# Performance work log

Measured on AMD Instinct MI355X. Metric: run time of the kernel, lower is better.

Reference implementation:

```python
import jax, jax.numpy as jnp
import numpy as np

EMBED_DIM = 256
NUM_EMBEDDINGS = 1024
COMMITMENT_COST = 0.25


def setup_inputs() -> dict:
    key = jax.random.key(0)
    k1, k2 = jax.random.split(key)
    z_e = jax.random.normal(k1, (64, 32, 32, EMBED_DIM), dtype=jnp.float32)
    # variance_scaling(fan_in, uniform) ~ U(-sqrt(3/fan_in), sqrt(3/fan_in))
    lim = float(np.sqrt(3.0 / EMBED_DIM))
    codebook = jax.random.uniform(k2, (NUM_EMBEDDINGS, EMBED_DIM), dtype=jnp.float32,
                                  minval=-lim, maxval=lim)
    return {"z_e": z_e, "codebook": codebook}


def reference(z_e, codebook):
    codebook = jnp.asarray(codebook, dtype=jnp.float32)
    z_flat = jnp.reshape(z_e, (-1, codebook.shape[1]))  # [N, D]
    # ||z||^2 - 2 z.c + ||c||^2 -> [N, K]
    distances = (jnp.sum(z_flat ** 2, axis=1, keepdims=True)
                 - 2.0 * jnp.dot(z_flat, codebook.T)
                 + jnp.sum(codebook ** 2, axis=1))
    encoding_indices = jnp.argmin(distances, axis=1)  # [N]
    quantized = jnp.reshape(codebook[encoding_indices], z_e.shape)
    commitment_loss = COMMITMENT_COST * jnp.mean((jax.lax.stop_gradient(quantized) - z_e) ** 2)
    embedding_loss = jnp.mean((quantized - jax.lax.stop_gradient(z_e)) ** 2)
    quantized = z_e + jax.lax.stop_gradient(quantized - z_e)  # straight-through
    return (quantized, commitment_loss, embedding_loss, encoding_indices)
```

## Files before the change

### kernel.cpp

```cpp
#include <hip/hip_runtime.h>

#define NROWS  65536
#define DIM    256
#define KCB    1024
#define DELTA  0.012f
#define DELTA2 2.0e-4f
#define NRMAX  65536

typedef __attribute__((ext_vector_type(8))) _Float16 v8h;
typedef __attribute__((ext_vector_type(4))) float v4f;
typedef __attribute__((ext_vector_type(4))) int   v4i;

__device__ __forceinline__ unsigned short h16(float x) {
  _Float16 h = (_Float16)x;
  return __builtin_bit_cast(unsigned short, h);
}
__device__ __forceinline__ unsigned pk2h(float a, float b) {
  return (unsigned)h16(a) | ((unsigned)h16(b) << 16);
}
__device__ __forceinline__ v4i pk8h(float4 a, float4 b) {
  v4i r; r.x = (int)pk2h(a.x,a.y); r.y = (int)pk2h(a.z,a.w);
  r.z = (int)pk2h(b.x,b.y); r.w = (int)pk2h(b.z,b.w);
  return r;
}
__device__ __forceinline__ float f16f(float x) { return (float)(_Float16)x; }
__device__ __forceinline__ void gld16(const void* g, void* l) {
  __builtin_amdgcn_global_load_lds(
      (const __attribute__((address_space(1))) unsigned int*)g,
      (__attribute__((address_space(3))) unsigned int*)l, 16, 0, 0);
}

__global__ __launch_bounds__(256) void prep_kernel(const float* __restrict__ cb,
                                                   float* __restrict__ cnorm,
                                                   unsigned short* __restrict__ cbh,
                                                   unsigned short* __restrict__ cbl,
                                                   int* __restrict__ cnt,
                                                   int* __restrict__ cnt2) {
  int g = blockIdx.x * 256 + threadIdx.x;
  if (g == 0) { *cnt = 0; *cnt2 = 0; }
  int k = g >> 2, q = g & 3;
  int nt = k >> 7, c = k & 127;
  const float4* row = reinterpret_cast<const float4*>(cb + (size_t)k * DIM) + q * 16;
  size_t off = (size_t)((nt * 4 + q) * 128 + c) * 64;
  unsigned short* dh = cbh + off;
  unsigned short* dl = cbl + off;
  int xr = (c & 7) << 3;
  double s = 0.0;
#pragma unroll
  for (int i = 0; i < 8; ++i) {
    float4 a = row[2 * i], b = row[2 * i + 1];
    s += (double)a.x * a.x + (double)a.y * a.y + (double)a.z * a.z + (double)a.w * a.w;
    s += (double)b.x * b.x + (double)b.y * b.y + (double)b.z * b.z + (double)b.w * b.w;
    *(v4i*)(dh + ((i * 8) ^ xr)) = pk8h(a, b);
    float4 ar, br;
    ar.x = a.x - f16f(a.x); ar.y = a.y - f16f(a.y);
    ar.z = a.z - f16f(a.z); ar.w = a.w - f16f(a.w);
    br.x = b.x - f16f(b.x); br.y = b.y - f16f(b.y);
    br.z = b.z - f16f(b.z); br.w = b.w - f16f(b.w);
    *(v4i*)(dl + ((i * 8) ^ xr)) = pk8h(ar, br);
  }
  s += __shfl_xor(s, 1);
  s += __shfl_xor(s, 2);
  if (q == 0) cnorm[k] = (float)s;
}

__global__ __launch_bounds__(256, 2) void vq_mfma(
    const float* __restrict__ z, const unsigned short* __restrict__ cbh,
    const float* __restrict__ cnw, int* __restrict__ idx_arr,
    int* __restrict__ list, int* __restrict__ cnt) {
  __shared__ __align__(16) short S[32768];

  const int t = threadIdx.x;
  const int l = t & 63;
  const int w = t >> 6;
  const int l15 = l & 15, lhi = l >> 4;
  const int wm = w * 32;
  const int r0 = blockIdx.x * 128;

#pragma unroll
  for (int p = 0; p < 16; ++p) {
    int u = t + p * 256;
    int row = u >> 5, k8 = u & 31;
    const float4* s = (const float4*)(z + (size_t)(r0 + row) * DIM + k8 * 8);
    float4 a = s[0], b = s[1];
    *(v4i*)(S + row * 256 + ((k8 * 8) ^ ((row & 7) << 3))) = pk8h(a, b);
  }
  __syncthreads();

  v8h A[2][8];
#pragma unroll
  for (int mf = 0; mf < 2; ++mf) {
    int arow = wm + mf * 16 + l15;
    int base = arow * 256, xr = (arow & 7) << 3;
#pragma unroll
    for (int ks8 = 0; ks8 < 8; ++ks8)
      A[mf][ks8] = *(const v8h*)(S + base + ((ks8 * 32 + lhi * 8) ^ xr));
  }
  __syncthreads();

  auto stageC = [&](int p) {
    const char* gb = (const char*)cbh + (size_t)p * 32768 + w * 8192 + l * 16;
    char* lb = (char*)(S + (p & 1) * 16384) + w * 8192;
#pragma unroll
    for (int j = 0; j < 8; ++j) gld16(gb + j * 1024, lb + j * 1024);
  };

  int bcode[8], boff[8], bxr[8];
#pragma unroll
  for (int nf = 0; nf < 8; ++nf) {
    bcode[nf] = nf * 16 + l15;
    boff[nf] = bcode[nf] * 64;
    bxr[nf] = (bcode[nf] & 7) << 3;
  }

  float m1[8], m2[8]; int i1[8];
#pragma unroll
  for (int sl = 0; sl < 8; ++sl) { m1[sl] = 3.0e38f; m2[sl] = 3.0e38f; i1[sl] = 0; }

  stageC(0);
  __syncthreads();

  for (int nt = 0; nt < 8; ++nt) {
    float cnv[8];
#pragma unroll
    for (int nf = 0; nf < 8; ++nf) cnv[nf] = cnw[nt * 128 + bcode[nf]];

    v4f acc[2][8];
#pragma unroll
    for (int mf = 0; mf < 2; ++mf)
#pragma unroll
      for (int nf = 0; nf < 8; ++nf) acc[mf][nf] = (v4f){0.f, 0.f, 0.f, 0.f};

    for (int kh = 0; kh < 2; ++kh) {
      int p = nt * 2 + kh;
      if (p < 15) stageC(p + 1);
      const short* cur = S + (p & 1) * 16384;
#pragma unroll
      for (int ks = 0; ks < 4; ++ks) {
        int sub = (ks >> 1) * 8192;
        int ko = (ks & 1) * 32 + lhi * 8;
        v8h b[8];
#pragma unroll
        for (int nf = 0; nf < 8; ++nf)
          b[nf] = *(const v8h*)(cur + sub + boff[nf] + (ko ^ bxr[nf]));
#pragma unroll
        for (int mf = 0; mf < 2; ++mf)
#pragma unroll
          for (int nf = 0; nf < 8; ++nf)
            acc[mf][nf] = __builtin_amdgcn_mfma_f32_16x16x32_f16(A[mf][kh * 4 + ks], b[nf], acc[mf][nf], 0, 0, 0);
      }
      __syncthreads();
    }

#pragma unroll
    for (int mf = 0; mf < 2; ++mf)
#pragma unroll
      for (int nf = 0; nf < 8; ++nf) {
        int code = nt * 128 + bcode[nf];
#pragma unroll
        for (int r = 0; r < 4; ++r) {
          float s = fmaf(-2.f, acc[mf][nf][r], cnv[nf]);
          int sl = mf * 4 + r;
          m2[sl] = fminf(m2[sl], fmaxf(m1[sl], s));
          bool lt = s < m1[sl];
          i1[sl] = lt ? code : i1[sl];
          m1[sl] = lt ? s : m1[sl];
        }
      }
  }

#pragma unroll
  for (int off = 1; off < 16; off <<= 1) {
#pragma unroll
    for (int sl = 0; sl < 8; ++sl) {
      float o1 = __shfl_xor(m1[sl], off);
      int   oi = __shfl_xor(i1[sl], off);
      float o2 = __shfl_xor(m2[sl], off);
      bool bb = (o1 < m1[sl]) || (o1 == m1[sl] && oi < i1[sl]);
      float hi = fmaxf(m1[sl], o1);
      m2[sl] = fminf(hi, fminf(m2[sl], o2));
      m1[sl] = bb ? o1 : m1[sl];
      i1[sl] = bb ? oi : i1[sl];
    }
  }

  if (l15 == 0) {
#pragma unroll
    for (int sl = 0; sl < 8; ++sl) {
      int row = wm + (sl >> 2) * 16 + lhi * 4 + (sl & 3);
      idx_arr[r0 + row] = i1[sl];
      if (m2[sl] - m1[sl] < DELTA) {
        int p = atomicAdd(cnt, 1);
        list[p] = r0 + row;
      }
    }
  }
}

__global__ __launch_bounds__(256, 2) void vq_refine(
    const float* __restrict__ z,
    const unsigned short* __restrict__ cbh, const unsigned short* __restrict__ cbl,
    const float* __restrict__ cnw, const int* __restrict__ list,
    const int* __restrict__ cnt,
    float* __restrict__ pm1, float* __restrict__ pm2, int* __restrict__ pi1) {
  __shared__ __align__(16) short Ch[2][8192];
  __shared__ __align__(16) short Cl[2][8192];
  __shared__ int rows_s[64];

  const int t = threadIdx.x;
  const int l = t & 63, w = t >> 6;
  const int l15 = l & 15, lhi = l >> 4;
  const int n = *cnt;
  const int ngroups = (n + 63) >> 6;
  const int cq = blockIdx.x & 3;

  auto stage2 = [&](int g, int buf) {
    size_t go = (size_t)g * 16384 + w * 4096 + l * 16;
    char* lh = (char*)Ch[buf] + w * 4096;
    char* ll = (char*)Cl[buf] + w * 4096;
#pragma unroll
    for (int j = 0; j < 4; ++j) gld16((const char*)cbh + go + j * 1024, lh + j * 1024);
#pragma unroll
    for (int j = 0; j < 4; ++j) gld16((const char*)cbl + go + j * 1024, ll + j * 1024);
  };

  const int bxr = (l15 & 7) << 3;

  for (int grp = blockIdx.x >> 2; grp < ngroups; grp += (gridDim.x >> 2)) {
    int base = grp * 64;
    __syncthreads();
    if (t < 64) rows_s[t] = list[min(base + t, n - 1)];
    __syncthreads();
    int rowg = rows_s[w * 16 + l15];

    v8h Ah[8], Al[8];
#pragma unroll
    for (int ks8 = 0; ks8 < 8; ++ks8) {
      const float* p = z + (size_t)rowg * 256 + ks8 * 32 + lhi * 8;
      float4 a = *(const float4*)p, b = *(const float4*)(p + 4);
      v8h hv, lv;
      hv[0] = (_Float16)a.x; lv[0] = (_Float16)(a.x - (float)hv[0]);
      hv[1] = (_Float16)a.y; lv[1] = (_Float16)(a.y - (float)hv[1]);
      hv[2] = (_Float16)a.z; lv[2] = (_Float16)(a.z - (float)hv[2]);
      hv[3] = (_Float16)a.w; lv[3] = (_Float16)(a.w - (float)hv[3]);
      hv[4] = (_Float16)b.x; lv[4] = (_Float16)(b.x - (float)hv[4]);
      hv[5] = (_Float16)b.y; lv[5] = (_Float16)(b.y - (float)hv[5]);
      hv[6] = (_Float16)b.z; lv[6] = (_Float16)(b.z - (float)hv[6]);
      hv[7] = (_Float16)b.w; lv[7] = (_Float16)(b.w - (float)hv[7]);
      Ah[ks8] = hv; Al[ks8] = lv;
    }

    stage2(cq * 8, 0);
    __syncthreads();

    float m1[4], m2[4]; int i1[4];
#pragma unroll
    for (int r = 0; r < 4; ++r) { m1[r] = 3.0e38f; m2[r] = 3.0e38f; i1[r] = 0; }

#pragma unroll
    for (int tnt = 0; tnt < 2; ++tnt) {
      int nt = cq * 2 + tnt;
      float cnv[8];
#pragma unroll
      for (int nf = 0; nf < 8; ++nf) cnv[nf] = cnw[nt * 128 + nf * 16 + l15];

      v4f acc[8];
#pragma unroll
      for (int nf = 0; nf < 8; ++nf) acc[nf] = (v4f){0.f, 0.f, 0.f, 0.f};

      for (int kc = 0; kc < 4; ++kc) {
        int ph = tnt * 4 + kc;
        int g = nt * 4 + kc;
        if (ph < 7) stage2(g + 1, (ph + 1) & 1);
        const short* ch = Ch[ph & 1];
        const short* cl = Cl[ph & 1];
#pragma unroll
        for (int ks = 0; ks < 2; ++ks) {
          int ko = (ks * 32 + lhi * 8) ^ bxr;
          v8h bh[8], bl8[8];
#pragma unroll
          for (int nf = 0; nf < 8; ++nf) {
            int bo = (nf * 16 + l15) * 64 + ko;
            bh[nf]  = *(const v8h*)(ch + bo);
            bl8[nf] = *(const v8h*)(cl + bo);
          }
          v8h ah = Ah[kc * 2 + ks], al = Al[kc * 2 + ks];
#pragma unroll
          for (int nf = 0; nf < 8; ++nf) {
            acc[nf] = __builtin_amdgcn_mfma_f32_16x16x32_f16(al, bh[nf], acc[nf], 0, 0, 0);
            acc[nf] = __builtin_amdgcn_mfma_f32_16x16x32_f16(ah, bl8[nf], acc[nf], 0, 0, 0);
            acc[nf] = __builtin_amdgcn_mfma_f32_16x16x32_f16(ah, bh[nf], acc[nf], 0, 0, 0);
          }
        }
        __syncthreads();
      }

#pragma unroll
      for (int nf = 0; nf < 8; ++nf) {
        int code = nt * 128 + nf * 16 + l15;
#pragma unroll
        for (int r = 0; r < 4; ++r) {
          float s = fmaf(-2.f, acc[nf][r], cnv[nf]);
          m2[r] = fminf(m2[r], fmaxf(m1[r], s));
          bool lt = s < m1[r];
          i1[r] = lt ? code : i1[r];
          m1[r] = lt ? s : m1[r];
        }
      }
    }

#pragma unroll
    for (int off = 1; off < 16; off <<= 1) {
#pragma unroll
      for (int r = 0; r < 4; ++r) {
        float o1 = __shfl_xor(m1[r], off);
        int   oi = __shfl_xor(i1[r], off);
        float o2 = __shfl_xor(m2[r], off);
        bool bb = (o1 < m1[r]) || (o1 == m1[r] && oi < i1[r]);
        float hi = fmaxf(m1[r], o1);
        m2[r] = fminf(hi, fminf(m2[r], o2));
        m1[r] = bb ? o1 : m1[r];
        i1[r] = bb ? oi : i1[r];
      }
    }

    if (l15 == 0) {
#pragma unroll
      for (int r = 0; r < 4; ++r) {
        int fr = w * 16 + lhi * 4 + r;
        int pos = base + fr;
        if (pos < n) {
          pm1[cq * NRMAX + pos] = m1[r];
          pm2[cq * NRMAX + pos] = m2[r];
          pi1[cq * NRMAX + pos] = i1[r];
        }
      }
    }
  }
}

__global__ __launch_bounds__(256) void vq_merge(
    const int* __restrict__ list, const int* __restrict__ cnt,
    const float* __restrict__ pm1, const float* __restrict__ pm2,
    const int* __restrict__ pi1, int* __restrict__ idx_arr,
    int* __restrict__ list2, int* __restrict__ cnt2) {
  int i = blockIdx.x * 256 + threadIdx.x;
  int n = *cnt;
  if (i >= n) return;
  float m1 = pm1[i], m2 = pm2[i];
  int   i1 = pi1[i];
#pragma unroll
  for (int cq = 1; cq < 4; ++cq) {
    float o1 = pm1[cq * NRMAX + i];
    float o2 = pm2[cq * NRMAX + i];
    int   oi = pi1[cq * NRMAX + i];
    bool bb = (o1 < m1) || (o1 == m1 && oi < i1);
    float hi = fmaxf(m1, o1);
    m2 = fminf(hi, fminf(m2, o2));
    m1 = bb ? o1 : m1;
    i1 = bb ? oi : i1;
  }
  int row = list[i];
  idx_arr[row] = i1;
  if (m2 - m1 < DELTA2) {
    int p = atomicAdd(cnt2, 1);
    list2[p] = row;
  }
}

__global__ __launch_bounds__(256) void vq_rescue(
    const float* __restrict__ z, const float* __restrict__ cb,
    const float* __restrict__ cnw, const int* __restrict__ list,
    const int* __restrict__ cnt, int* __restrict__ idx_arr) {
  __shared__ float zs[256];
  __shared__ float As;
  __shared__ float wmin[4];
  __shared__ int   widx[4];

  const int t = threadIdx.x;
  const int l = t & 63, w = t >> 6;
  const int n = *cnt;

  for (int i = blockIdx.x; i < n; i += gridDim.x) {
    int row = list[i];
    __syncthreads();
    if (t < 64) ((float4*)zs)[t] = ((const float4*)(z + (size_t)row * DIM))[t];
    __syncthreads();
    if (t < 4) {
      double s = 0.0;
      const float* zz = zs + t * 64;
      for (int d = 0; d < 64; ++d) { float v = zz[d]; s += (double)v * v; }
      s += __shfl_xor(s, 1);
      s += __shfl_xor(s, 2);
      if (t == 0) As = (float)s;
    }
    __syncthreads();
    float Af = As;

    const float4* c0 = (const float4*)(cb + (size_t)(t      ) * DIM);
    const float4* c1 = (const float4*)(cb + (size_t)(t + 256) * DIM);
    const float4* c2 = (const float4*)(cb + (size_t)(t + 512) * DIM);
    const float4* c3 = (const float4*)(cb + (size_t)(t + 768) * DIM);
    float a0 = 0.f, a1 = 0.f, a2 = 0.f, a3 = 0.f;
    for (int d4 = 0; d4 < 64; ++d4) {
      float4 zq = *(const float4*)(zs + d4 * 4);
      float4 va = c0[d4], vb = c1[d4], vc = c2[d4], vd = c3[d4];
      a0 = fmaf(zq.x, va.x, a0); a0 = fmaf(zq.y, va.y, a0);
      a0 = fmaf(zq.z, va.z, a0); a0 = fmaf(zq.w, va.w, a0);
      a1 = fmaf(zq.x, vb.x, a1); a1 = fmaf(zq.y, vb.y, a1);
      a1 = fmaf(zq.z, vb.z, a1); a1 = fmaf(zq.w, vb.w, a1);
      a2 = fmaf(zq.x, vc.x, a2); a2 = fmaf(zq.y, vc.y, a2);
      a2 = fmaf(zq.z, vc.z, a2); a2 = fmaf(zq.w, vc.w, a2);
      a3 = fmaf(zq.x, vd.x, a3); a3 = fmaf(zq.y, vd.y, a3);
      a3 = fmaf(zq.z, vd.z, a3); a3 = fmaf(zq.w, vd.w, a3);
    }
    float accs[4] = {a0, a1, a2, a3};
    float mv = 3.0e38f; int mi = 0;
#pragma unroll
    for (int j = 0; j < 4; ++j) {
      int code = t + j * 256;
      float t1 = fmaf(-2.f, accs[j], Af);
      float t2 = t1 + cnw[code];
      if (t2 < mv) { mv = t2; mi = code; }
    }
#pragma unroll
    for (int off = 1; off < 64; off <<= 1) {
      float ov = __shfl_xor(mv, off);
      int   oi = __shfl_xor(mi, off);
      if (ov < mv || (ov == mv && oi < mi)) { mv = ov; mi = oi; }
    }
    if (l == 0) { wmin[w] = mv; widx[w] = mi; }
    __syncthreads();
    if (t == 0) {
      float bm = wmin[0]; int bi = widx[0];
#pragma unroll
      for (int q = 1; q < 4; ++q)
        if (wmin[q] < bm || (wmin[q] == bm && widx[q] < bi)) { bm = wmin[q]; bi = widx[q]; }
      idx_arr[row] = bi;
    }
    __syncthreads();
  }
}

__global__ __launch_bounds__(256) void vq_epilogue(
    const float* __restrict__ z, const float* __restrict__ cb,
    const int* __restrict__ idx_arr, float* __restrict__ out_q,
    float* __restrict__ out_idx, double* __restrict__ partial) {
  __shared__ int idxs[16];
  __shared__ double lw[4];
  const int t = threadIdx.x;
  const int b0 = blockIdx.x * 16;
  if (t < 16) {
    int k = idx_arr[b0 + t];
    idxs[t] = k;
    out_idx[b0 + t] = (float)k;
  }
  __syncthreads();
  const float4* zb = (const float4*)(z + (size_t)b0 * DIM);
  float4* qb = (float4*)(out_q + (size_t)b0 * DIM);
  double ls = 0.0;
#pragma unroll
  for (int p = 0; p < 4; ++p) {
    int fi = p * 256 + t;
    int ki = idxs[fi >> 6];
    float4 zv = zb[fi];
    float4 cv = ((const float4*)(cb + (size_t)ki * DIM))[fi & 63];
    float dx = cv.x - zv.x, dy = cv.y - zv.y, dz = cv.z - zv.z, dw = cv.w - zv.w;
    float4 o; o.x = zv.x + dx; o.y = zv.y + dy; o.z = zv.z + dz; o.w = zv.w + dw;
    qb[fi] = o;
    ls += (double)dx * dx + (double)dy * dy + (double)dz * dz + (double)dw * dw;
  }
#pragma unroll
  for (int off = 1; off < 64; off <<= 1) ls += __shfl_xor(ls, off);
  if ((t & 63) == 0) lw[t >> 6] = ls;
  __syncthreads();
  if (t == 0) partial[blockIdx.x] = lw[0] + lw[1] + lw[2] + lw[3];
}

__global__ __launch_bounds__(256) void finalize_kernel(const double* __restrict__ partial,
                                                       float* __restrict__ out_losses) {
  __shared__ double lw[4];
  const int t = threadIdx.x;
  double s = 0.0;
  for (int i = t; i < 4096; i += 256) s += partial[i];
#pragma unroll
  for (int off = 1; off < 64; off <<= 1) s += __shfl_xor(s, off);
  if ((t & 63) == 0) lw[t >> 6] = s;
  __syncthreads();
  if (t == 0) {
    double mse = (lw[0] + lw[1] + lw[2] + lw[3]) / ((double)NROWS * (double)DIM);
    out_losses[0] = (float)(0.25 * mse);
    out_losses[1] = (float)mse;
  }
}

extern "C" void kernel_launch(void* const* d_in, const int* in_sizes, int n_in,
                              void* d_out, int out_size, void* d_ws, size_t ws_size,
                              hipStream_t stream) {
  const float* z  = (const float*)d_in[0];
  const float* cb = (const float*)d_in[1];
  float* out = (float*)d_out;

  char* ws = (char*)d_ws;
  int*            cnt     = (int*)(ws + 0);
  int*            cnt2    = (int*)(ws + 8);
  float*          cnorm   = (float*)(ws + 4096);
  double*         partial = (double*)(ws + 8192);
  int*            idx_arr = (int*)(ws + 40960);
  int*            list    = (int*)(ws + 303104);
  int*            list2   = (int*)(ws + 565248);
  unsigned short* cbh     = (unsigned short*)(ws + 827392);
  unsigned short* cbl     = (unsigned short*)(ws + 1351680);
  float*          pm1     = (float*)(ws + 1875968);
  float*          pm2     = (float*)(ws + 2924544);
  int*            pi1     = (int*)(ws + 3973120);

  float* out_q      = out;
  float* out_losses = out + 16777216;
  float* out_idx    = out + 16777218;

  prep_kernel<<<16, 256, 0, stream>>>(cb, cnorm, cbh, cbl, cnt, cnt2);
  vq_mfma<<<NROWS / 128, 256, 0, stream>>>(z, cbh, cnorm, idx_arr, list, cnt);
  vq_refine<<<1024, 256, 0, stream>>>(z, cbh, cbl, cnorm, list, cnt, pm1, pm2, pi1);
  vq_merge<<<NRMAX / 256, 256, 0, stream>>>(list, cnt, pm1, pm2, pi1, idx_arr, list2, cnt2);
  vq_rescue<<<256, 256, 0, stream>>>(z, cb, cnorm, list2, cnt2, idx_arr);
  vq_epilogue<<<NROWS / 16, 256, 0, stream>>>(z, cb, idx_arr, out_q, out_idx, partial);
  finalize_kernel<<<1, 256, 0, stream>>>(partial, out_losses);
}
```

Measured before the change: 166.8 us.

## Fuse epilogue into refine kernel and patch only ambiguous rows afterwards

Merges the refine pass and the full epilogue into one launch: the first 1024 blocks refine ambiguous rows while the remaining blocks write quantized outputs and per-row losses from the coarse indices. A small patch kernel then rewrites output and loss for the listed rows whose index may have changed. The losses now go into a per-row float buffer that finalize sums. The aim is to overlap the memory-bound epilogue with the compute-bound refine and drop one full-size pass. The cost is that listed rows get written twice, and each per-row loss is rounded to float before summation.

```diff
diff --git a/kernel.cpp b/kernel.cpp
--- a/kernel.cpp
+++ b/kernel.cpp
@@ -6,6 +6,7 @@
 #define DELTA  0.012f
 #define DELTA2 2.0e-4f
 #define NRMAX  65536
+#define REFB   1024
 
 typedef __attribute__((ext_vector_type(8))) _Float16 v8h;
 typedef __attribute__((ext_vector_type(4))) float v4f;
@@ -197,144 +198,175 @@
   }
 }
 
-__global__ __launch_bounds__(256, 2) void vq_refine(
-    const float* __restrict__ z,
+__global__ __launch_bounds__(256, 2) void vq_fused(
+    const float* __restrict__ z, const float* __restrict__ cb,
     const unsigned short* __restrict__ cbh, const unsigned short* __restrict__ cbl,
     const float* __restrict__ cnw, const int* __restrict__ list,
-    const int* __restrict__ cnt,
-    float* __restrict__ pm1, float* __restrict__ pm2, int* __restrict__ pi1) {
+    const int* __restrict__ cnt, const int* __restrict__ idx_arr,
+    float* __restrict__ pm1, float* __restrict__ pm2, int* __restrict__ pi1,
+    float* __restrict__ out_q, float* __restrict__ out_idx,
+    float* __restrict__ rowloss) {
   __shared__ __align__(16) short Ch[2][8192];
   __shared__ __align__(16) short Cl[2][8192];
   __shared__ int rows_s[64];
+  __shared__ int idxs[16];
 
   const int t = threadIdx.x;
   const int l = t & 63, w = t >> 6;
   const int l15 = l & 15, lhi = l >> 4;
-  const int n = *cnt;
-  const int ngroups = (n + 63) >> 6;
-  const int cq = blockIdx.x & 3;
-
-  auto stage2 = [&](int g, int buf) {
-    size_t go = (size_t)g * 16384 + w * 4096 + l * 16;
-    char* lh = (char*)Ch[buf] + w * 4096;
-    char* ll = (char*)Cl[buf] + w * 4096;
-#pragma unroll
-    for (int j = 0; j < 4; ++j) gld16((const char*)cbh + go + j * 1024, lh + j * 1024);
-#pragma unroll
-    for (int j = 0; j < 4; ++j) gld16((const char*)cbl + go + j * 1024, ll + j * 1024);
-  };
-
-  const int bxr = (l15 & 7) << 3;
-
-  for (int grp = blockIdx.x >> 2; grp < ngroups; grp += (gridDim.x >> 2)) {
-    int base = grp * 64;
-    __syncthreads();
-    if (t < 64) rows_s[t] = list[min(base + t, n - 1)];
-    __syncthreads();
-    int rowg = rows_s[w * 16 + l15];
-
-    v8h Ah[8], Al[8];
-#pragma unroll
-    for (int ks8 = 0; ks8 < 8; ++ks8) {
-      const float* p = z + (size_t)rowg * 256 + ks8 * 32 + lhi * 8;
-      float4 a = *(const float4*)p, b = *(const float4*)(p + 4);
-      v8h hv, lv;
-      hv[0] = (_Float16)a.x; lv[0] = (_Float16)(a.x - (float)hv[0]);
-      hv[1] = (_Float16)a.y; lv[1] = (_Float16)(a.y - (float)hv[1]);
-      hv[2] = (_Float16)a.z; lv[2] = (_Float16)(a.z - (float)hv[2]);
-      hv[3] = (_Float16)a.w; lv[3] = (_Float16)(a.w - (float)hv[3]);
-      hv[4] = (_Float16)b.x; lv[4] = (_Float16)(b.x - (float)hv[4]);
-      hv[5] = (_Float16)b.y; lv[5] = (_Float16)(b.y - (float)hv[5]);
-      hv[6] = (_Float16)b.z; lv[6] = (_Float16)(b.z - (float)hv[6]);
-      hv[7] = (_Float16)b.w; lv[7] = (_Float16)(b.w - (float)hv[7]);
-      Ah[ks8] = hv; Al[ks8] = lv;
-    }
-
-    stage2(cq * 8, 0);
-    __syncthreads();
-
-    float m1[4], m2[4]; int i1[4];
-#pragma unroll
-    for (int r = 0; r < 4; ++r) { m1[r] = 3.0e38f; m2[r] = 3.0e38f; i1[r] = 0; }
-
-#pragma unroll
-    for (int tnt = 0; tnt < 2; ++tnt) {
-      int nt = cq * 2 + tnt;
-      float cnv[8];
-#pragma unroll
-      for (int nf = 0; nf < 8; ++nf) cnv[nf] = cnw[nt * 128 + nf * 16 + l15];
-
-      v4f acc[8];
-#pragma unroll
-      for (int nf = 0; nf < 8; ++nf) acc[nf] = (v4f){0.f, 0.f, 0.f, 0.f};
-
-      for (int kc = 0; kc < 4; ++kc) {
-        int ph = tnt * 4 + kc;
-        int g = nt * 4 + kc;
-        if (ph < 7) stage2(g + 1, (ph + 1) & 1);
-        const short* ch = Ch[ph & 1];
-        const short* cl = Cl[ph & 1];
-#pragma unroll
-        for (int ks = 0; ks < 2; ++ks) {
-          int ko = (ks * 32 + lhi * 8) ^ bxr;
-          v8h bh[8], bl8[8];
-#pragma unroll
-          for (int nf = 0; nf < 8; ++nf) {
-            int bo = (nf * 16 + l15) * 64 + ko;
-            bh[nf]  = *(const v8h*)(ch + bo);
-            bl8[nf] = *(const v8h*)(cl + bo);
+
+  if (blockIdx.x < REFB) {
+    const int n = *cnt;
+    const int ngroups = (n + 63) >> 6;
+    const int cq = blockIdx.x & 3;
+
+    auto stage2 = [&](int g, int buf) {
+      size_t go = (size_t)g * 16384 + w * 4096 + l * 16;
+      char* lh = (char*)Ch[buf] + w * 4096;
+      char* ll = (char*)Cl[buf] + w * 4096;
+#pragma unroll
+      for (int j = 0; j < 4; ++j) gld16((const char*)cbh + go + j * 1024, lh + j * 1024);
+#pragma unroll
+      for (int j = 0; j < 4; ++j) gld16((const char*)cbl + go + j * 1024, ll + j * 1024);
+    };
+
+    const int bxr = (l15 & 7) << 3;
+
+    for (int grp = blockIdx.x >> 2; grp < ngroups; grp += (REFB >> 2)) {
+      int base = grp * 64;
+      __syncthreads();
+      if (t < 64) rows_s[t] = list[min(base + t, n - 1)];
+      __syncthreads();
+      int rowg = rows_s[w * 16 + l15];
+
+      v8h Ah[8], Al[8];
+#pragma unroll
+      for (int ks8 = 0; ks8 < 8; ++ks8) {
+        const float* p = z + (size_t)rowg * 256 + ks8 * 32 + lhi * 8;
+        float4 a = *(const float4*)p, b = *(const float4*)(p + 4);
+        v8h hv, lv;
+        hv[0] = (_Float16)a.x; lv[0] = (_Float16)(a.x - (float)hv[0]);
+        hv[1] = (_Float16)a.y; lv[1] = (_Float16)(a.y - (float)hv[1]);
+        hv[2] = (_Float16)a.z; lv[2] = (_Float16)(a.z - (float)hv[2]);
+        hv[3] = (_Float16)a.w; lv[3] = (_Float16)(a.w - (float)hv[3]);
+        hv[4] = (_Float16)b.x; lv[4] = (_Float16)(b.x - (float)hv[4]);
+        hv[5] = (_Float16)b.y; lv[5] = (_Float16)(b.y - (float)hv[5]);
+        hv[6] = (_Float16)b.z; lv[6] = (_Float16)(b.z - (float)hv[6]);
+        hv[7] = (_Float16)b.w; lv[7] = (_Float16)(b.w - (float)hv[7]);
+        Ah[ks8] = hv; Al[ks8] = lv;
+      }
+
+      stage2(cq * 8, 0);
+      __syncthreads();
+
+      float m1[4], m2[4]; int i1[4];
+#pragma unroll
+      for (int r = 0; r < 4; ++r) { m1[r] = 3.0e38f; m2[r] = 3.0e38f; i1[r] = 0; }
+
+#pragma unroll
+      for (int tnt = 0; tnt < 2; ++tnt) {
+        int nt = cq * 2 + tnt;
+        float cnv[8];
+#pragma unroll
+        for (int nf = 0; nf < 8; ++nf) cnv[nf] = cnw[nt * 128 + nf * 16 + l15];
+
+        v4f acc[8];
+#pragma unroll
+        for (int nf = 0; nf < 8; ++nf) acc[nf] = (v4f){0.f, 0.f, 0.f, 0.f};
+
+        for (int kc = 0; kc < 4; ++kc) {
+          int ph = tnt * 4 + kc;
+          int g = nt * 4 + kc;
+          if (ph < 7) stage2(g + 1, (ph + 1) & 1);
+          const short* ch = Ch[ph & 1];
+          const short* cl = Cl[ph & 1];
+#pragma unroll
+          for (int ks = 0; ks < 2; ++ks) {
+            int ko = (ks * 32 + lhi * 8) ^ bxr;
+            v8h bh[8], bl8[8];
+#pragma unroll
+            for (int nf = 0; nf < 8; ++nf) {
+              int bo = (nf * 16 + l15) * 64 + ko;
+              bh[nf]  = *(const v8h*)(ch + bo);
+              bl8[nf] = *(const v8h*)(cl + bo);
+            }
+            v8h ah = Ah[kc * 2 + ks], al = Al[kc * 2 + ks];
+#pragma unroll
+            for (int nf = 0; nf < 8; ++nf) {
+              acc[nf] = __builtin_amdgcn_mfma_f32_16x16x32_f16(al, bh[nf], acc[nf], 0, 0, 0);
+              acc[nf] = __builtin_amdgcn_mfma_f32_16x16x32_f16(ah, bl8[nf], acc[nf], 0, 0, 0);
+              acc[nf] = __builtin_amdgcn_mfma_f32_16x16x32_f16(ah, bh[nf], acc[nf], 0, 0, 0);
+            }
           }
-          v8h ah = Ah[kc * 2 + ks], al = Al[kc * 2 + ks];
-#pragma unroll
-          for (int nf = 0; nf < 8; ++nf) {
-            acc[nf] = __builtin_amdgcn_mfma_f32_16x16x32_f16(al, bh[nf], acc[nf], 0, 0, 0);
-            acc[nf] = __builtin_amdgcn_mfma_f32_16x16x32_f16(ah, bl8[nf], acc[nf], 0, 0, 0);
-            acc[nf] = __builtin_amdgcn_mfma_f32_16x16x32_f16(ah, bh[nf], acc[nf], 0, 0, 0);
+          __syncthreads();
+        }
+
+#pragma unroll
+        for (int nf = 0; nf < 8; ++nf) {
+          int code = nt * 128 + nf * 16 + l15;
+#pragma unroll
+          for (int r = 0; r < 4; ++r) {
+            float s = fmaf(-2.f, acc[nf][r], cnv[nf]);
+            m2[r] = fminf(m2[r], fmaxf(m1[r], s));
+            bool lt = s < m1[r];
+            i1[r] = lt ? code : i1[r];
+            m1[r] = lt ? s : m1[r];
           }
         }
-        __syncthreads();
-      }
-
-#pragma unroll
-      for (int nf = 0; nf < 8; ++nf) {
-        int code = nt * 128 + nf * 16 + l15;
+      }
+
+#pragma unroll
+      for (int off = 1; off < 16; off <<= 1) {
 #pragma unroll
         for (int r = 0; r < 4; ++r) {
-          float s = fmaf(-2.f, acc[nf][r], cnv[nf]);
-          m2[r] = fminf(m2[r], fmaxf(m1[r], s));
-          bool lt = s < m1[r];
-          i1[r] = lt ? code : i1[r];
-          m1[r] = lt ? s : m1[r];
+          float o1 = __shfl_xor(m1[r], off);
+          int   oi = __shfl_xor(i1[r], off);
+          float o2 = __shfl_xor(m2[r], off);
+          bool bb = (o1 < m1[r]) || (o1 == m1[r] && oi < i1[r]);
+          float hi = fmaxf(m1[r], o1);
+          m2[r] = fminf(hi, fminf(m2[r], o2));
+          m1[r] = bb ? o1 : m1[r];
+          i1[r] = bb ? oi : i1[r];
         }
       }
-    }
-
-#pragma unroll
-    for (int off = 1; off < 16; off <<= 1) {
-#pragma unroll
-      for (int r = 0; r < 4; ++r) {
-        float o1 = __shfl_xor(m1[r], off);
-        int   oi = __shfl_xor(i1[r], off);
-        float o2 = __shfl_xor(m2[r], off);
-        bool bb = (o1 < m1[r]) || (o1 == m1[r] && oi < i1[r]);
-        float hi = fmaxf(m1[r], o1);
-        m2[r] = fminf(hi, fminf(m2[r], o2));
-        m1[r] = bb ? o1 : m1[r];
-        i1[r] = bb ? oi : i1[r];
-      }
-    }
-
-    if (l15 == 0) {
-#pragma unroll
-      for (int r = 0; r < 4; ++r) {
-        int fr = w * 16 + lhi * 4 + r;
-        int pos = base + fr;
-        if (pos < n) {
-          pm1[cq * NRMAX + pos] = m1[r];
-          pm2[cq * NRMAX + pos] = m2[r];
-          pi1[cq * NRMAX + pos] = i1[r];
+
+      if (l15 == 0) {
+#pragma unroll
+        for (int r = 0; r < 4; ++r) {
+          int fr = w * 16 + lhi * 4 + r;
+          int pos = base + fr;
+          if (pos < n) {
+            pm1[cq * NRMAX + pos] = m1[r];
+            pm2[cq * NRMAX + pos] = m2[r];
+            pi1[cq * NRMAX + pos] = i1[r];
+          }
         }
       }
+    }
+  } else {
+    const int b0 = (blockIdx.x - REFB) * 16;
+    if (t < 16) {
+      int k = idx_arr[b0 + t];
+      idxs[t] = k;
+      out_idx[b0 + t] = (float)k;
+    }
+    __syncthreads();
+    const float4* zb = (const float4*)(z + (size_t)b0 * DIM);
+    float4* qb = (float4*)(out_q + (size_t)b0 * DIM);
+#pragma unroll
+    for (int p = 0; p < 4; ++p) {
+      int rl = p * 4 + w;
+      int fi = p * 256 + t;
+      int ki = idxs[rl];
+      float4 zv = zb[fi];
+      float4 cv = ((const float4*)(cb + (size_t)ki * DIM))[fi & 63];
+      float dx = cv.x - zv.x, dy = cv.y - zv.y, dz = cv.z - zv.z, dw = cv.w - zv.w;
+      float4 o; o.x = zv.x + dx; o.y = zv.y + dy; o.z = zv.z + dz; o.w = zv.w + dw;
+      qb[fi] = o;
+      double ls = (double)dx * dx + (double)dy * dy + (double)dz * dz + (double)dw * dw;
+#pragma unroll
+      for (int off = 1; off < 64; off <<= 1) ls += __shfl_xor(ls, off);
+      if (l == 0) rowloss[b0 + rl] = (float)ls;
     }
   }
 }
@@ -442,47 +474,37 @@
   }
 }
 
-__global__ __launch_bounds__(256) void vq_epilogue(
+__global__ __launch_bounds__(64) void vq_patch(
     const float* __restrict__ z, const float* __restrict__ cb,
+    const int* __restrict__ list, const int* __restrict__ cnt,
     const int* __restrict__ idx_arr, float* __restrict__ out_q,
-    float* __restrict__ out_idx, double* __restrict__ partial) {
-  __shared__ int idxs[16];
-  __shared__ double lw[4];
-  const int t = threadIdx.x;
-  const int b0 = blockIdx.x * 16;
-  if (t < 16) {
-    int k = idx_arr[b0 + t];
-    idxs[t] = k;
-    out_idx[b0 + t] = (float)k;
-  }
-  __syncthreads();
-  const float4* zb = (const float4*)(z + (size_t)b0 * DIM);
-  float4* qb = (float4*)(out_q + (size_t)b0 * DIM);
-  double ls = 0.0;
-#pragma unroll
-  for (int p = 0; p < 4; ++p) {
-    int fi = p * 256 + t;
-    int ki = idxs[fi >> 6];
-    float4 zv = zb[fi];
-    float4 cv = ((const float4*)(cb + (size_t)ki * DIM))[fi & 63];
+    float* __restrict__ out_idx, float* __restrict__ rowloss) {
+  const int l = threadIdx.x;
+  const int n = *cnt;
+  for (int i = blockIdx.x; i < n; i += gridDim.x) {
+    int row = list[i];
+    int k = idx_arr[row];
+    float4 zv = ((const float4*)(z + (size_t)row * DIM))[l];
+    float4 cv = ((const float4*)(cb + (size_t)k * DIM))[l];
     float dx = cv.x - zv.x, dy = cv.y - zv.y, dz = cv.z - zv.z, dw = cv.w - zv.w;
     float4 o; o.x = zv.x + dx; o.y = zv.y + dy; o.z = zv.z + dz; o.w = zv.w + dw;
-    qb[fi] = o;
-    ls += (double)dx * dx + (double)dy * dy + (double)dz * dz + (double)dw * dw;
-  }
-#pragma unroll
-  for (int off = 1; off < 64; off <<= 1) ls += __shfl_xor(ls, off);
-  if ((t & 63) == 0) lw[t >> 6] = ls;
-  __syncthreads();
-  if (t == 0) partial[blockIdx.x] = lw[0] + lw[1] + lw[2] + lw[3];
-}
-
-__global__ __launch_bounds__(256) void finalize_kernel(const double* __restrict__ partial,
+    ((float4*)(out_q + (size_t)row * DIM))[l] = o;
+    double ls = (double)dx * dx + (double)dy * dy + (double)dz * dz + (double)dw * dw;
+#pragma unroll
+    for (int off = 1; off < 64; off <<= 1) ls += __shfl_xor(ls, off);
+    if (l == 0) { rowloss[row] = (float)ls; out_idx[row] = (float)k; }
+  }
+}
+
+__global__ __launch_bounds__(256) void finalize_kernel(const float* __restrict__ rowloss,
                                                        float* __restrict__ out_losses) {
   __shared__ double lw[4];
   const int t = threadIdx.x;
   double s = 0.0;
-  for (int i = t; i < 4096; i += 256) s += partial[i];
+  for (int i = t; i < NROWS / 4; i += 256) {
+    float4 v = ((const float4*)rowloss)[i];
+    s += (double)v.x + (double)v.y + (double)v.z + (double)v.w;
+  }
 #pragma unroll
   for (int off = 1; off < 64; off <<= 1) s += __shfl_xor(s, off);
   if ((t & 63) == 0) lw[t >> 6] = s;
@@ -505,15 +527,15 @@
   int*            cnt     = (int*)(ws + 0);
   int*            cnt2    = (int*)(ws + 8);
   float*          cnorm   = (float*)(ws + 4096);
-  double*         partial = (double*)(ws + 8192);
-  int*            idx_arr = (int*)(ws + 40960);
-  int*            list    = (int*)(ws + 303104);
-  int*            list2   = (int*)(ws + 565248);
-  unsigned short* cbh     = (unsigned short*)(ws + 827392);
-  unsigned short* cbl     = (unsigned short*)(ws + 1351680);
-  float*          pm1     = (float*)(ws + 1875968);
-  float*          pm2     = (float*)(ws + 2924544);
-  int*            pi1     = (int*)(ws + 3973120);
+  float*          rowloss = (float*)(ws + 8192);
+  int*            idx_arr = (int*)(ws + 270336);
+  int*            list    = (int*)(ws + 532480);
+  int*            list2   = (int*)(ws + 794624);
+  unsigned short* cbh     = (unsigned short*)(ws + 1056768);
+  unsigned short* cbl     = (unsigned short*)(ws + 1581056);
+  float*          pm1     = (float*)(ws + 2105344);
+  float*          pm2     = (float*)(ws + 3153920);
+  int*            pi1     = (int*)(ws + 4202496);
 
   float* out_q      = out;
   float* out_losses = out + 16777216;
@@ -521,9 +543,11 @@
 
   prep_kernel<<<16, 256, 0, stream>>>(cb, cnorm, cbh, cbl, cnt, cnt2);
   vq_mfma<<<NROWS / 128, 256, 0, stream>>>(z, cbh, cnorm, idx_arr, list, cnt);
-  vq_refine<<<1024, 256, 0, stream>>>(z, cbh, cbl, cnorm, list, cnt, pm1, pm2, pi1);
+  vq_fused<<<REFB + NROWS / 16, 256, 0, stream>>>(z, cb, cbh, cbl, cnorm, list, cnt,
+                                                  idx_arr, pm1, pm2, pi1,
+                                                  out_q, out_idx, rowloss);
   vq_merge<<<NRMAX / 256, 256, 0, stream>>>(list, cnt, pm1, pm2, pi1, idx_arr, list2, cnt2);
   vq_rescue<<<256, 256, 0, stream>>>(z, cb, cnorm, list2, cnt2, idx_arr);
-  vq_epilogue<<<NROWS / 16, 256, 0, stream>>>(z, cb, idx_arr, out_q, out_idx, partial);
-  finalize_kernel<<<1, 256, 0, stream>>>(partial, out_losses);
-}
+  vq_patch<<<1024, 64, 0, stream>>>(z, cb, list, cnt, idx_arr, out_q, out_idx, rowloss);
+  finalize_kernel<<<1, 256, 0, stream>>>(rowloss, out_losses);
+}
```

After: 166.3 us. Within noise of the previous version (-0.3%).
